# Optimization experiments

Measured on AMD Instinct MI355X. Metric: run time of the kernel, lower is better.

Reference implementation:

```python
import jax, jax.numpy as jnp
import numpy as np

N, T, D, H = 6144, 3072, 128, 4
ALPHA = 0.2
NEG = -9e15


def mhgat(x, mask, W, a_src, a_dst, fc_W, fc_b):
    # x: [n, D], mask: [n, n] (0/1), W: [H, D, D], a_src/a_dst: [H, D]
    Wh = jnp.einsum('nd,hde->hne', x, W)                      # [H, n, D]
    f_s = jnp.einsum('hne,he->hn', Wh, a_src)                 # [H, n]
    f_d = jnp.einsum('hne,he->hn', Wh, a_dst)                 # [H, n]
    e = jax.nn.leaky_relu(f_s[:, :, None] + f_d[:, None, :], ALPHA)  # [H, n, n]
    scores = jnp.where(mask[None, :, :] > 0, e, NEG)
    attn = jax.nn.softmax(scores, axis=-1)                    # masked softmax over neighbors
    h = jnp.einsum('hnm,hme->hne', attn, Wh)                  # [H, n, D]
    h = jax.nn.elu(h)                                         # concat=True -> elu per head
    h = jnp.transpose(h, (1, 0, 2)).reshape(x.shape[0], H * h.shape[-1])  # [n, H*D]
    return jax.nn.relu(h @ fc_W + fc_b)                       # fully_connectedLyer = Linear+ReLU


def setup_inputs() -> dict:
    key = jax.random.key(0)
    ks = jax.random.split(key, 20)
    s = 0.05
    return {
        'x': jax.random.normal(ks[0], (N, D), jnp.float32),
        'adj': jax.random.randint(ks[1], (N, N), 0, 2, jnp.int32),
        't_x': jax.random.normal(ks[2], (T, D), jnp.float32),
        't_adj': jax.random.randint(ks[3], (T, T), 0, 2, jnp.int32),
        'tfidf_x': jax.random.uniform(ks[4], (T, N), jnp.float32),
        # concept-graph MHGAT params
        'Wg': jax.random.normal(ks[5], (H, D, D), jnp.float32) * s,
        'ag_src': jax.random.normal(ks[6], (H, D), jnp.float32) * s,
        'ag_dst': jax.random.normal(ks[7], (H, D), jnp.float32) * s,
        'fcg_W': jax.random.normal(ks[8], (H * D, D), jnp.float32) * s,
        'fcg_b': jnp.zeros((D,), jnp.float32),
        # text-graph MHGAT params
        'Wt': jax.random.normal(ks[9], (H, D, D), jnp.float32) * s,
        'at_src': jax.random.normal(ks[10], (H, D), jnp.float32) * s,
        'at_dst': jax.random.normal(ks[11], (H, D), jnp.float32) * s,
        'fct_W': jax.random.normal(ks[12], (H * D, D), jnp.float32) * s,
        'fct_b': jnp.zeros((D,), jnp.float32),
        # fusion fc params
        'fus_W': jax.random.normal(ks[13], (D, D), jnp.float32) * s,
        'fus_b': jnp.zeros((D,), jnp.float32),
    }


def reference(x, adj, t_x, t_adj, tfidf_x,
              Wg, ag_src, ag_dst, fcg_W, fcg_b,
              Wt, at_src, at_dst, fct_W, fct_b,
              fus_W, fus_b):
    concept = mhgat(x, adj, Wg, ag_src, ag_dst, fcg_W, fcg_b)        # [N, D]
    gat_text = mhgat(t_x, t_adj, Wt, at_src, at_dst, fct_W, fct_b)   # [T, D]
    c_text = tfidf_x.T @ gat_text                                    # [N, D]
    z = jax.nn.sigmoid(concept + c_text)
    fusion = z * concept + (1.0 - z) * c_text
    return jax.nn.relu(fusion @ fus_W + fus_b)
```

## Files before the change

kernel.cpp:

```cpp
#include <hip/hip_runtime.h>
#include <hip/hip_bf16.h>
#include <stdint.h>

#define N_  6144
#define T_  3072
#define D_  128
#define H_  4
#define HD_ 512

typedef float f32x4 __attribute__((ext_vector_type(4)));
typedef short s16x8 __attribute__((ext_vector_type(8)));
typedef _Float16 h16x4 __attribute__((ext_vector_type(4)));

#define GLL16(g, s) __builtin_amdgcn_global_load_lds( \
    (const __attribute__((address_space(1))) unsigned int*)(g), \
    (__attribute__((address_space(3))) unsigned int*)(s), 16, 0, 0)

static __device__ __forceinline__ short f2bf(float f) {
  union { __hip_bfloat16 b; short s; } u;
  u.b = __float2bfloat16(f);
  return u.s;
}

__global__ __launch_bounds__(256) void bits8_kernel(const int* __restrict__ a0,
                                                    const int* __restrict__ a1,
                                                    unsigned long long* __restrict__ b0,
                                                    unsigned long long* __restrict__ b1,
                                                    int nw0, int nw1) {
  int lane = threadIdx.x & 63;
  int gw = (blockIdx.x * blockDim.x + threadIdx.x) >> 6;
  int nw = (gridDim.x * blockDim.x) >> 6;
  int total8 = (nw0 + nw1) >> 3;
  for (int g = gw; g < total8; g += nw) {
    int w = g * 8;
    const int* src; unsigned long long* dst; long wi;
    if (w < nw0) { src = a0; dst = b0; wi = w; }
    else         { src = a1; dst = b1; wi = w - nw0; }
    int v[8];
#pragma unroll
    for (int j = 0; j < 8; ++j) v[j] = src[(wi + j) * 64 + lane];
    unsigned long long bb[8];
#pragma unroll
    for (int j = 0; j < 8; ++j) bb[j] = __ballot(v[j] != 0);
    if (lane == 0) {
      ulonglong2 s01 = {bb[0], bb[1]}, s23 = {bb[2], bb[3]};
      ulonglong2 s45 = {bb[4], bb[5]}, s67 = {bb[6], bb[7]};
      *(ulonglong2*)(dst + wi + 0) = s01;
      *(ulonglong2*)(dst + wi + 2) = s23;
      *(ulonglong2*)(dst + wi + 4) = s45;
      *(ulonglong2*)(dst + wi + 6) = s67;
    }
  }
}

__global__ __launch_bounds__(256) void cvt2_kernel(const float* __restrict__ in0,
                                                   short* __restrict__ out0,
                                                   const float* __restrict__ in1,
                                                   short* __restrict__ out1,
                                                   int c0, int c1) {
  int i = blockIdx.x * blockDim.x + threadIdx.x;
  const float* in; short* out; long ii;
  if (i < c0) { in = in0; out = out0; ii = i; }
  else if (i < c0 + c1) { in = in1; out = out1; ii = i - c0; }
  else return;
  float4 v = *(const float4*)(in + ii * 4);
  short4 o;
  o.x = f2bf(v.x); o.y = f2bf(v.y); o.z = f2bf(v.z); o.w = f2bf(v.w);
  *(short4*)(out + ii * 4) = o;
}

__global__ __launch_bounds__(256) void tcvt2_kernel(const float* __restrict__ in0,
                                                    short* __restrict__ out0,
                                                    const float* __restrict__ in1,
                                                    short* __restrict__ out1,
                                                    int R, int C, long sIn, long sOut,
                                                    int zsplit) {
  __shared__ float t[32][33];
  const float* in; short* out;
  int z = blockIdx.z;
  if (z < zsplit) { in = in0 + (long)z * sIn; out = out0 + (long)z * sOut; }
  else            { in = in1 + (long)(z - zsplit) * sIn; out = out1 + (long)(z - zsplit) * sOut; }
  int c0 = blockIdx.x * 32, r0 = blockIdx.y * 32;
  int tx = threadIdx.x, ty = threadIdx.y;
#pragma unroll
  for (int i = 0; i < 4; ++i)
    t[ty + 8 * i][tx] = in[(long)(r0 + ty + 8 * i) * C + c0 + tx];
  __syncthreads();
#pragma unroll
  for (int i = 0; i < 4; ++i)
    out[(long)(c0 + ty + 8 * i) * R + r0 + tx] = f2bf(t[tx][ty + 8 * i]);
}

__global__ __launch_bounds__(256) void fvec_kernel(const float* __restrict__ x,
                                                   const float* __restrict__ W,
                                                   const float* __restrict__ a_s,
                                                   const float* __restrict__ a_d,
                                                   float* __restrict__ ea, float* __restrict__ ec,
                                                   float* __restrict__ inv,
                                                   float* __restrict__ eb, float* __restrict__ ed,
                                                   int n) {
  __shared__ float usl[128], udl[128], asl[128], adl[128];
  long idx = (long)blockIdx.x * 256 + threadIdx.x;
  int h = (int)(idx / n), i = (int)(idx % n);
  int tid = threadIdx.x;
  if (tid < 128) {
    asl[tid] = a_s[h * D_ + tid];
    adl[tid] = a_d[h * D_ + tid];
  }
  __syncthreads();
  {
    int d = tid & 127;
    const float* wr = W + ((long)h * D_ + d) * D_;
    const float* av = (tid < 128) ? asl : adl;
    float s = 0.f;
#pragma unroll 8
    for (int e = 0; e < D_; ++e) s += wr[e] * av[e];
    if (tid < 128) usl[d] = s; else udl[d] = s;
  }
  __syncthreads();
  const float4* xr = (const float4*)(x + (long)i * D_);
  float s = 0.f, t = 0.f;
#pragma unroll 8
  for (int e4 = 0; e4 < 32; ++e4) {
    float4 xv = xr[e4];
    s += xv.x * usl[4 * e4] + xv.y * usl[4 * e4 + 1] + xv.z * usl[4 * e4 + 2] + xv.w * usl[4 * e4 + 3];
    t += xv.x * udl[4 * e4] + xv.y * udl[4 * e4 + 1] + xv.z * udl[4 * e4 + 2] + xv.w * udl[4 * e4 + 3];
  }
  const float L2E = 1.4426950408889634f;
  float fs = s * L2E, fd = t * L2E;
  ea[idx]  = exp2f(fs);
  ec[idx]  = exp2f(0.2f * fs);
  inv[idx] = exp2f(-fs);
  eb[idx]  = exp2f(fd);
  ed[idx]  = exp2f(0.2f * fd);
}

__global__ __launch_bounds__(256) void gemm_kernel(const short* __restrict__ A,
                                                   const short* __restrict__ BT,
                                                   int K, int lda, int ldb,
                                                   float* __restrict__ outF, short* __restrict__ outB,
                                                   int ldo, int epi,
                                                   long sA, long sBT, long sOut) {
  int bz = blockIdx.z;
  A += bz * sA;
  BT += bz * sBT;
  __shared__ __align__(16) short bs[2][4096];
  int tid = threadIdx.x, w = tid >> 6, l = tid & 63, lm = l & 15, lg = l >> 4;
  int row0 = blockIdx.x * 64 + w * 16;
  int col0 = blockIdx.y * 128;
  const short* arow = A + (long)(row0 + lm) * lda + 8 * lg;
  const short* bsrc = BT + (long)(col0 + 16 * (2 * w) + lm) * ldb + 8 * lg;
  f32x4 acc[8] = {};
  int nt = K / 32;
  s16x8 af = *(const s16x8*)(arow);
  GLL16(bsrc, &bs[0][(2 * w) * 512]);
  GLL16(bsrc + 16 * ldb, &bs[0][(2 * w + 1) * 512]);
  for (int kt = 0; kt < nt; ++kt) {
    int cur = kt & 1, nxt = cur ^ 1;
    int kb = (kt + 1 < nt ? kt + 1 : kt) * 32;
    s16x8 an = *(const s16x8*)(arow + kb);
    asm volatile("s_waitcnt vmcnt(1)" ::: "memory");
    __builtin_amdgcn_sched_barrier(0);
    __builtin_amdgcn_s_barrier();
    __builtin_amdgcn_sched_barrier(0);
#pragma unroll
    for (int f = 0; f < 8; ++f) {
      s16x8 bf = *(const s16x8*)(&bs[cur][f * 512 + l * 8]);
      acc[f] = __builtin_amdgcn_mfma_f32_16x16x32_bf16(af, bf, acc[f], 0, 0, 0);
    }
    if (kt + 1 < nt) {
      GLL16(bsrc + kb, &bs[nxt][(2 * w) * 512]);
      GLL16(bsrc + kb + 16 * ldb, &bs[nxt][(2 * w + 1) * 512]);
    }
    __builtin_amdgcn_sched_barrier(0);
    af = an;
  }
#pragma unroll
  for (int f = 0; f < 8; ++f) {
    int col = col0 + 16 * f + lm;
#pragma unroll
    for (int r = 0; r < 4; ++r) {
      int row = row0 + 4 * lg + r;
      if (epi == 0) outB[bz * sOut + (long)row * ldo + col] = f2bf(acc[f][r]);
      else          outF[bz * sOut + (long)row * ldo + col] = acc[f][r];
    }
  }
}

__global__ __launch_bounds__(256) void reduce_kernel(const float* __restrict__ P,
                                                     int S, long sP,
                                                     const float* __restrict__ bias,
                                                     short* __restrict__ outB,
                                                     int ldo) {
  __shared__ short sm[128][68];
  int tid = threadIdx.x;
  int r0 = blockIdx.x * 64;
#pragma unroll
  for (int k = 0; k < 8; ++k) {
    int e = tid * 4 + k * 1024;
    int row = e >> 7, col = e & 127;
    f32x4 v = {};
    for (int s = 0; s < S; ++s)
      v += *(const f32x4*)(P + (long)s * sP + (long)(r0 + row) * 128 + col);
    const float4 bv = *(const float4*)(bias + col);
    v[0] += bv.x; v[1] += bv.y; v[2] += bv.z; v[3] += bv.w;
#pragma unroll
    for (int q = 0; q < 4; ++q) v[q] = v[q] > 0.f ? v[q] : 0.f;
    sm[col + 0][row] = f2bf(v[0]);
    sm[col + 1][row] = f2bf(v[1]);
    sm[col + 2][row] = f2bf(v[2]);
    sm[col + 3][row] = f2bf(v[3]);
  }
  __syncthreads();
  int d = tid >> 1, seg = tid & 1;
  short* dst = outB + (long)d * ldo + r0 + seg * 32;
#pragma unroll
  for (int q = 0; q < 8; ++q) {
    short4 o;
    o.x = sm[d][seg * 32 + 4 * q + 0];
    o.y = sm[d][seg * 32 + 4 * q + 1];
    o.z = sm[d][seg * 32 + 4 * q + 2];
    o.w = sm[d][seg * 32 + 4 * q + 3];
    *(short4*)(dst + 4 * q) = o;
  }
}

__global__ __launch_bounds__(256) void attn_kernel(const short* __restrict__ WhT,
                                                   const unsigned char* __restrict__ bits,
                                                   const float* __restrict__ eaA,
                                                   const float* __restrict__ ecA,
                                                   const float* __restrict__ invA,
                                                   const float* __restrict__ ebA,
                                                   const float* __restrict__ edA,
                                                   _Float16* __restrict__ pacc,
                                                   float* __restrict__ pz,
                                                   int n, int S) {
  int h = blockIdx.y, sp = blockIdx.z;
  int RB = gridDim.x;
  int klen = n / S, k0 = sp * klen;
  const short* whT = WhT + (long)h * D_ * n;
  const float* ebp = ebA + (long)h * n;
  const float* edp = edA + (long)h * n;
  __shared__ __align__(16) short bs[2][4096];
  int tid = threadIdx.x, w = tid >> 6, l = tid & 63, lm = l & 15, lg = l >> 4;
  int i0 = blockIdx.x * 128;
  int r0 = i0 + 32 * w + lm;
  int r1 = r0 + 16;
  float ea0 = eaA[(long)h * n + r0], ea1 = eaA[(long)h * n + r1];
  float ec0 = ecA[(long)h * n + r0], ec1 = ecA[(long)h * n + r1];
  float iv0 = invA[(long)h * n + r0], iv1 = invA[(long)h * n + r1];
  const unsigned char* brow0 = bits + (long)r0 * (n >> 3);
  const unsigned char* brow1 = bits + (long)r1 * (n >> 3);
  const short* bsrc = whT + (long)(16 * (2 * w) + lm) * n + 8 * lg + k0;
  f32x4 acc0[8] = {}, acc1[8] = {};
  f32x4 az0 = {}, az1 = {};
  s16x8 ones;
#pragma unroll
  for (int j = 0; j < 8; ++j) ones[j] = (short)0x3F80;
  int nt = klen / 32;
  float ebR[8], edR[8], ebS[8], edS[8];
  unsigned m0A, m1A, m0B, m1B;
  *(float4*)(ebR)     = *(const float4*)(ebp + k0 + 8 * lg);
  *(float4*)(ebR + 4) = *(const float4*)(ebp + k0 + 8 * lg + 4);
  *(float4*)(edR)     = *(const float4*)(edp + k0 + 8 * lg);
  *(float4*)(edR + 4) = *(const float4*)(edp + k0 + 8 * lg + 4);
  m0A = (*(const unsigned*)(brow0 + (k0 >> 3))) >> (8 * lg);
  m1A = (*(const unsigned*)(brow1 + (k0 >> 3))) >> (8 * lg);
  GLL16(bsrc, &bs[0][(2 * w) * 512]);
  GLL16(bsrc + 16 * n, &bs[0][(2 * w + 1) * 512]);

#define ATTN_STEP(KT, EBC, EDC, M0C, M1C, EBN, EDN, M0N, M1N)                   \
  {                                                                             \
    int cur = (KT) & 1, nxt = cur ^ 1;                                          \
    int kb = ((KT) + 1 < nt ? (KT) + 1 : (KT)) * 32;                            \
    *(float4*)(EBN)     = *(const float4*)(ebp + k0 + kb + 8 * lg);             \
    *(float4*)(EBN + 4) = *(const float4*)(ebp + k0 + kb + 8 * lg + 4);         \
    *(float4*)(EDN)     = *(const float4*)(edp + k0 + kb + 8 * lg);             \
    *(float4*)(EDN + 4) = *(const float4*)(edp + k0 + kb + 8 * lg + 4);         \
    M0N = (*(const unsigned*)(brow0 + ((k0 + kb) >> 3))) >> (8 * lg);           \
    M1N = (*(const unsigned*)(brow1 + ((k0 + kb) >> 3))) >> (8 * lg);           \
    union { s16x8 v; unsigned u[4]; } af0, af1;                                 \
    _Pragma("unroll")                                                           \
    for (int jj = 0; jj < 4; ++jj) {                                            \
      float bva = EBC[2 * jj], bvb = EBC[2 * jj + 1];                           \
      float dva = EDC[2 * jj], dvb = EDC[2 * jj + 1];                           \
      int ta = ((int)(M0C << (31 - 2 * jj))) >> 31;                             \
      int tb = ((int)(M0C << (30 - 2 * jj))) >> 31;                             \
      bool ca = bva > iv0, cb = bvb > iv0;                                      \
      float pa = (ca ? bva : dva) * (ca ? ea0 : ec0);                           \
      float pb = (cb ? bvb : dvb) * (cb ? ea0 : ec0);                           \
      pa = __int_as_float(ta & __float_as_int(pa));                             \
      pb = __int_as_float(tb & __float_as_int(pb));                             \
      af0.u[jj] = __builtin_amdgcn_perm(__float_as_uint(pb) + 0x8000u,          \
                                        __float_as_uint(pa) + 0x8000u, 0x07060302); \
      ta = ((int)(M1C << (31 - 2 * jj))) >> 31;                                 \
      tb = ((int)(M1C << (30 - 2 * jj))) >> 31;                                 \
      ca = bva > iv1; cb = bvb > iv1;                                           \
      pa = (ca ? bva : dva) * (ca ? ea1 : ec1);                                 \
      pb = (cb ? bvb : dvb) * (cb ? ea1 : ec1);                                 \
      pa = __int_as_float(ta & __float_as_int(pa));                             \
      pb = __int_as_float(tb & __float_as_int(pb));                             \
      af1.u[jj] = __builtin_amdgcn_perm(__float_as_uint(pb) + 0x8000u,          \
                                        __float_as_uint(pa) + 0x8000u, 0x07060302); \
    }                                                                           \
    asm volatile("s_waitcnt vmcnt(6)" ::: "memory");                            \
    __builtin_amdgcn_sched_barrier(0);                                          \
    __builtin_amdgcn_s_barrier();                                               \
    __builtin_amdgcn_sched_barrier(0);                                          \
    _Pragma("unroll")                                                           \
    for (int f = 0; f < 8; ++f) {                                               \
      s16x8 bf = *(const s16x8*)(&bs[cur][f * 512 + l * 8]);                    \
      acc0[f] = __builtin_amdgcn_mfma_f32_16x16x32_bf16(af0.v, bf, acc0[f], 0, 0, 0); \
      acc1[f] = __builtin_amdgcn_mfma_f32_16x16x32_bf16(af1.v, bf, acc1[f], 0, 0, 0); \
    }                                                                           \
    az0 = __builtin_amdgcn_mfma_f32_16x16x32_bf16(af0.v, ones, az0, 0, 0, 0);   \
    az1 = __builtin_amdgcn_mfma_f32_16x16x32_bf16(af1.v, ones, az1, 0, 0, 0);   \
    if ((KT) + 1 < nt) {                                                        \
      GLL16(bsrc + kb, &bs[nxt][(2 * w) * 512]);                                \
      GLL16(bsrc + kb + 16 * n, &bs[nxt][(2 * w + 1) * 512]);                   \
    }                                                                           \
    __builtin_amdgcn_sched_barrier(0);                                          \
  }

  for (int kt = 0; kt < nt; kt += 2) {
    ATTN_STEP(kt,     ebR, edR, m0A, m1A, ebS, edS, m0B, m1B);
    ATTN_STEP(kt + 1, ebS, edS, m0B, m1B, ebR, edR, m0A, m1A);
  }
#undef ATTN_STEP

  long base = (long)(h * RB + blockIdx.x) * S + sp;
  if (lm == 0) {
#pragma unroll
    for (int r = 0; r < 4; ++r) {
      pz[base * 128 + 32 * w + 4 * lg + r] = az0[r];
      pz[base * 128 + 32 * w + 16 + 4 * lg + r] = az1[r];
    }
  }
  long pb = base * 16384;
#pragma unroll
  for (int f = 0; f < 8; ++f)
#pragma unroll
    for (int r = 0; r < 4; ++r) {
      pacc[pb + (long)(32 * w + 4 * lg + r) * 128 + 16 * f + lm] = (_Float16)acc0[f][r];
      pacc[pb + (long)(32 * w + 16 + 4 * lg + r) * 128 + 16 * f + lm] = (_Float16)acc1[f][r];
    }
}

__global__ __launch_bounds__(256) void attn_combine_kernel(const _Float16* __restrict__ pacc,
                                                           const float* __restrict__ pz,
                                                           short* __restrict__ hcat,
                                                           int S) {
  int h = blockIdx.y, rb = blockIdx.x;
  int RB = gridDim.x;
  long base = (long)(h * RB + rb) * S;
  __shared__ float zl[128];
  int tid = threadIdx.x;
  if (tid < 128) {
    float zv = 0.f;
    for (int s = 0; s < S; ++s) zv += pz[(base + s) * 128 + tid];
    zl[tid] = 1.f / zv;
  }
  __syncthreads();
  int i0 = rb * 128;
#pragma unroll
  for (int k = 0; k < 16; ++k) {
    int e = tid * 4 + k * 1024;
    int row = e >> 7, col = e & 127;
    f32x4 v = {};
    for (int s = 0; s < S; ++s) {
      h16x4 hv = *(const h16x4*)(pacc + (base + s) * 16384 + e);
      v[0] += (float)hv[0]; v[1] += (float)hv[1];
      v[2] += (float)hv[2]; v[3] += (float)hv[3];
    }
    float iz = zl[row];
    short4 o;
    float t;
    t = v[0] * iz; o.x = f2bf(t > 0.f ? t : __expf(t) - 1.f);
    t = v[1] * iz; o.y = f2bf(t > 0.f ? t : __expf(t) - 1.f);
    t = v[2] * iz; o.z = f2bf(t > 0.f ? t : __expf(t) - 1.f);
    t = v[3] * iz; o.w = f2bf(t > 0.f ? t : __expf(t) - 1.f);
    *(short4*)(hcat + (long)(i0 + row) * HD_ + h * D_ + col) = o;
  }
}

__global__ __launch_bounds__(256) void fusion_kernel(const float* __restrict__ fcPg,
                                                     int Sf, long sPg,
                                                     const float* __restrict__ fcg_b,
                                                     const float* __restrict__ ctextP,
                                                     int Sc, long sCt,
                                                     const short* __restrict__ fusT,
                                                     const float* __restrict__ fus_b,
                                                     float* __restrict__ out) {
  __shared__ __align__(16) short als[64 * 136];
  int tid = threadIdx.x;
  int r0 = blockIdx.x * 64;
#pragma unroll
  for (int it = 0; it < 8; ++it) {
    int e = it * 1024 + tid * 4;
    int r = e >> 7, c = e & 127;
    f32x4 cv = {};
    for (int s = 0; s < Sf; ++s)
      cv += *(const f32x4*)(fcPg + (long)s * sPg + (long)(r0 + r) * D_ + c);
    const float4 bv = *(const float4*)(fcg_b + c);
    cv[0] += bv.x; cv[1] += bv.y; cv[2] += bv.z; cv[3] += bv.w;
#pragma unroll
    for (int q = 0; q < 4; ++q) cv[q] = cv[q] > 0.f ? cv[q] : 0.f;
    f32x4 tv = {};
    for (int s = 0; s < Sc; ++s)
      tv += *(const f32x4*)(ctextP + (long)s * sCt + (long)(r0 + r) * D_ + c);
    short4 o;
    {
      float s0 = cv[0] + tv[0]; float z = 1.f / (1.f + __expf(-s0)); o.x = f2bf(tv[0] + z * (cv[0] - tv[0]));
      s0 = cv[1] + tv[1]; z = 1.f / (1.f + __expf(-s0)); o.y = f2bf(tv[1] + z * (cv[1] - tv[1]));
      s0 = cv[2] + tv[2]; z = 1.f / (1.f + __expf(-s0)); o.z = f2bf(tv[2] + z * (cv[2] - tv[2]));
      s0 = cv[3] + tv[3]; z = 1.f / (1.f + __expf(-s0)); o.w = f2bf(tv[3] + z * (cv[3] - tv[3]));
    }
    *(short4*)(als + (long)r * 136 + c) = o;
  }
  __syncthreads();
  int w = tid >> 6, l = tid & 63, lm = l & 15, lg = l >> 4;
  f32x4 acc[8] = {};
#pragma unroll
  for (int kt = 0; kt < 4; ++kt) {
    int kb = kt * 32;
    s16x8 af = *(const s16x8*)(als + (16 * w + lm) * 136 + kb + 8 * lg);
#pragma unroll
    for (int f = 0; f < 8; ++f) {
      s16x8 bf = *(const s16x8*)(fusT + (long)(16 * f + lm) * D_ + kb + 8 * lg);
      acc[f] = __builtin_amdgcn_mfma_f32_16x16x32_bf16(af, bf, acc[f], 0, 0, 0);
    }
  }
#pragma unroll
  for (int f = 0; f < 8; ++f) {
    int col = 16 * f + lm;
#pragma unroll
    for (int r = 0; r < 4; ++r) {
      float v = acc[f][r] + fus_b[col];
      v = v > 0.f ? v : 0.f;
      out[(long)(r0 + 16 * w + 4 * lg + r) * D_ + col] = v;
    }
  }
}

extern "C" void kernel_launch(void* const* d_in, const int* in_sizes, int n_in,
                              void* d_out, int out_size, void* d_ws, size_t ws_size,
                              hipStream_t stream) {
  (void)in_sizes; (void)n_in; (void)out_size;
  const float* x      = (const float*)d_in[0];
  const int*   adj    = (const int*)d_in[1];
  const float* t_x    = (const float*)d_in[2];
  const int*   t_adj  = (const int*)d_in[3];
  const float* tfidf  = (const float*)d_in[4];
  const float* Wg     = (const float*)d_in[5];
  const float* ag_src = (const float*)d_in[6];
  const float* ag_dst = (const float*)d_in[7];
  const float* fcg_W  = (const float*)d_in[8];
  const float* fcg_b  = (const float*)d_in[9];
  const float* Wt     = (const float*)d_in[10];
  const float* at_src = (const float*)d_in[11];
  const float* at_dst = (const float*)d_in[12];
  const float* fct_W  = (const float*)d_in[13];
  const float* fct_b  = (const float*)d_in[14];
  const float* fus_W  = (const float*)d_in[15];
  const float* fus_b  = (const float*)d_in[16];
  float* out = (float*)d_out;

  char* ws = (char*)d_ws;
  size_t off = 0;
  auto alloc = [&](size_t bytes) -> char* {
    char* p = ws + off;
    off = (off + bytes + 255) & ~(size_t)255;
    return p;
  };
  unsigned long long* bitsG = (unsigned long long*)alloc((size_t)N_ * N_ / 8);
  unsigned long long* bitsT = (unsigned long long*)alloc((size_t)T_ * T_ / 8);
  short* xb     = (short*)alloc((size_t)N_ * D_ * 2);
  short* txb    = (short*)alloc((size_t)T_ * D_ * 2);
  short* WgT    = (short*)alloc((size_t)H_ * D_ * D_ * 2);
  short* WtT    = (short*)alloc((size_t)H_ * D_ * D_ * 2);
  short* fcgT   = (short*)alloc((size_t)HD_ * D_ * 2);
  short* fctT   = (short*)alloc((size_t)HD_ * D_ * 2);
  short* fusT   = (short*)alloc((size_t)D_ * D_ * 2);
  short* tfidfT = (short*)alloc((size_t)N_ * T_ * 2);
  short* WhTg   = (short*)alloc((size_t)H_ * D_ * N_ * 2);
  short* WhTt   = (short*)alloc((size_t)H_ * D_ * T_ * 2);
  float* eaG  = (float*)alloc((size_t)H_ * N_ * 4);
  float* ecG  = (float*)alloc((size_t)H_ * N_ * 4);
  float* invG = (float*)alloc((size_t)H_ * N_ * 4);
  float* ebG  = (float*)alloc((size_t)H_ * N_ * 4);
  float* edG  = (float*)alloc((size_t)H_ * N_ * 4);
  float* eaT  = (float*)alloc((size_t)H_ * T_ * 4);
  float* ecT  = (float*)alloc((size_t)H_ * T_ * 4);
  float* invT = (float*)alloc((size_t)H_ * T_ * 4);
  float* ebT  = (float*)alloc((size_t)H_ * T_ * 4);
  float* edT  = (float*)alloc((size_t)H_ * T_ * 4);
  short* hcatG = (short*)alloc((size_t)N_ * HD_ * 2);
  short* hcatT = (short*)alloc((size_t)T_ * HD_ * 2);
  short* gatT  = (short*)alloc((size_t)D_ * T_ * 2);

  const int RBg = N_ / 128, RBt = T_ / 128;
  const size_t paccG1 = (size_t)H_ * RBg * 16384 * 2;
  const size_t paccT1 = (size_t)H_ * RBt * 16384 * 2;
  const size_t pzG1   = (size_t)H_ * RBg * 128 * 4;
  const size_t pzT1   = (size_t)H_ * RBt * 128 * 4;
  const size_t fcPg1  = (size_t)N_ * D_ * 4;
  const size_t fcPt1  = (size_t)T_ * D_ * 4;
  const size_t ctp1   = (size_t)N_ * D_ * 4;
  size_t rem = (ws_size > off + (1 << 20)) ? (ws_size - off - (1 << 20)) : 0;
  int Sg = 2, St = 2, Sf = 1, Sc = 1;
  size_t needFull = 8 * (paccG1 + pzG1) + 8 * (paccT1 + pzT1) + 4 * fcPg1 + 4 * fcPt1 + 4 * ctp1;
  size_t needMid  = 4 * (paccG1 + pzG1) + 4 * (paccT1 + pzT1) + 2 * fcPg1 + 2 * fcPt1 + 2 * ctp1;
  if (rem >= needFull)      { Sg = 8; St = 8; Sf = 4; Sc = 4; }
  else if (rem >= needMid)  { Sg = 4; St = 4; Sf = 2; Sc = 2; }
  _Float16* paccG = (_Float16*)alloc(Sg * paccG1);
  float* pzG   = (float*)alloc(Sg * pzG1);
  _Float16* paccT = (_Float16*)alloc(St * paccT1);
  float* pzT   = (float*)alloc(St * pzT1);
  float* fcPg  = (float*)alloc(Sf * fcPg1);
  float* fcPt  = (float*)alloc(Sf * fcPt1);
  float* ctextP = (float*)alloc(Sc * ctp1);

  bits8_kernel<<<dim3(1536), dim3(256), 0, stream>>>(adj, t_adj, bitsG, bitsT,
                                                     N_ * N_ / 64, T_ * T_ / 64);
  cvt2_kernel<<<dim3((N_ + T_) * D_ / 1024), dim3(256), 0, stream>>>(
      x, xb, t_x, txb, N_ * D_ / 4, T_ * D_ / 4);
  tcvt2_kernel<<<dim3(4, 4, 8), dim3(32, 8), 0, stream>>>(
      Wg, WgT, Wt, WtT, D_, D_, (long)D_ * D_, (long)D_ * D_, 4);
  tcvt2_kernel<<<dim3(4, 16, 2), dim3(32, 8), 0, stream>>>(
      fcg_W, fcgT, fct_W, fctT, HD_, D_, 0, 0, 1);
  tcvt2_kernel<<<dim3(4, 4, 1), dim3(32, 8), 0, stream>>>(
      fus_W, fusT, fus_W, fusT, D_, D_, 0, 0, 1);
  tcvt2_kernel<<<dim3(N_ / 32, T_ / 32, 1), dim3(32, 8), 0, stream>>>(
      tfidf, tfidfT, tfidf, tfidfT, T_, N_, 0, 0, 1);
  fvec_kernel<<<dim3(H_ * N_ / 256), dim3(256), 0, stream>>>(
      x, Wg, ag_src, ag_dst, eaG, ecG, invG, ebG, edG, N_);
  fvec_kernel<<<dim3(H_ * T_ / 256), dim3(256), 0, stream>>>(
      t_x, Wt, at_src, at_dst, eaT, ecT, invT, ebT, edT, T_);

  gemm_kernel<<<dim3(2, N_ / 128, H_), dim3(256), 0, stream>>>(
      WgT, xb, D_, D_, D_, nullptr, WhTg, N_, 0, (long)D_ * D_, 0, (long)D_ * N_);
  gemm_kernel<<<dim3(2, T_ / 128, H_), dim3(256), 0, stream>>>(
      WtT, txb, D_, D_, D_, nullptr, WhTt, T_, 0, (long)D_ * D_, 0, (long)D_ * T_);

  attn_kernel<<<dim3(RBg, H_, Sg), dim3(256), 0, stream>>>(
      WhTg, (const unsigned char*)bitsG, eaG, ecG, invG, ebG, edG, paccG, pzG, N_, Sg);
  attn_combine_kernel<<<dim3(RBg, H_), dim3(256), 0, stream>>>(paccG, pzG, hcatG, Sg);
  attn_kernel<<<dim3(RBt, H_, St), dim3(256), 0, stream>>>(
      WhTt, (const unsigned char*)bitsT, eaT, ecT, invT, ebT, edT, paccT, pzT, T_, St);
  attn_combine_kernel<<<dim3(RBt, H_), dim3(256), 0, stream>>>(paccT, pzT, hcatT, St);

  gemm_kernel<<<dim3(N_ / 64, 1, Sf), dim3(256), 0, stream>>>(
      hcatG, fcgT, HD_ / Sf, HD_, HD_, fcPg, nullptr, D_, 3,
      (long)(HD_ / Sf), (long)(HD_ / Sf), (long)N_ * D_);
  gemm_kernel<<<dim3(T_ / 64, 1, Sf), dim3(256), 0, stream>>>(
      hcatT, fctT, HD_ / Sf, HD_, HD_, fcPt, nullptr, D_, 3,
      (long)(HD_ / Sf), (long)(HD_ / Sf), (long)T_ * D_);
  reduce_kernel<<<dim3(T_ / 64), dim3(256), 0, stream>>>(
      fcPt, Sf, (long)T_ * D_, fct_b, gatT, T_);

  gemm_kernel<<<dim3(N_ / 64, 1, Sc), dim3(256), 0, stream>>>(
      tfidfT, gatT, T_ / Sc, T_, T_, ctextP, nullptr, D_, 3,
      (long)(T_ / Sc), (long)(T_ / Sc), (long)N_ * D_);

  fusion_kernel<<<dim3(N_ / 64), dim3(256), 0, stream>>>(
      fcPg, Sf, (long)N_ * D_, fcg_b, ctextP, Sc, (long)N_ * D_, fusT, fus_b, out);
}
```

Measured before the change: 392.4 us.

## Switch pipeline to fp16 MFMA with packed-half attention weights and triple buffering

Converts all bf16 intermediates and MFMA calls to fp16. The attention weight computation now uses packed half-precision multiply and max (max(ea*eb, ec*ed) replacing the compare-and-select leaky-relu), which drops the inv array and halves eb/ed storage. The gemm and attention kernels move from double to triple buffering with two-ahead global-to-LDS prefetch. Split-K factors are also changed. This carries fp16 overflow/precision risk for the exponentials and uses more shared memory per block.

```diff
diff --git a/kernel.cpp b/kernel.cpp
--- a/kernel.cpp
+++ b/kernel.cpp
@@ -9,17 +9,32 @@
 #define HD_ 512
 
 typedef float f32x4 __attribute__((ext_vector_type(4)));
-typedef short s16x8 __attribute__((ext_vector_type(8)));
+typedef _Float16 f16x8 __attribute__((ext_vector_type(8)));
 typedef _Float16 h16x4 __attribute__((ext_vector_type(4)));
 
 #define GLL16(g, s) __builtin_amdgcn_global_load_lds( \
     (const __attribute__((address_space(1))) unsigned int*)(g), \
     (__attribute__((address_space(3))) unsigned int*)(s), 16, 0, 0)
 
-static __device__ __forceinline__ short f2bf(float f) {
-  union { __hip_bfloat16 b; short s; } u;
-  u.b = __float2bfloat16(f);
+static __device__ __forceinline__ short f2h(float f) {
+  union { _Float16 h; short s; } u;
+  u.h = (_Float16)f;
   return u.s;
+}
+static __device__ __forceinline__ unsigned pk2(float f) {
+  union { _Float16 h[2]; unsigned u; } t;
+  t.h[0] = (_Float16)f; t.h[1] = t.h[0];
+  return t.u;
+}
+static __device__ __forceinline__ unsigned pkmul(unsigned a, unsigned b) {
+  unsigned r;
+  asm("v_pk_mul_f16 %0, %1, %2" : "=v"(r) : "v"(a), "v"(b));
+  return r;
+}
+static __device__ __forceinline__ unsigned pkmax(unsigned a, unsigned b) {
+  unsigned r;
+  asm("v_pk_max_f16 %0, %1, %2" : "=v"(r) : "v"(a), "v"(b));
+  return r;
 }
 
 __global__ __launch_bounds__(256) void bits8_kernel(const int* __restrict__ a0,
@@ -65,7 +80,7 @@
   else return;
   float4 v = *(const float4*)(in + ii * 4);
   short4 o;
-  o.x = f2bf(v.x); o.y = f2bf(v.y); o.z = f2bf(v.z); o.w = f2bf(v.w);
+  o.x = f2h(v.x); o.y = f2h(v.y); o.z = f2h(v.z); o.w = f2h(v.w);
   *(short4*)(out + ii * 4) = o;
 }
 
@@ -88,7 +103,7 @@
   __syncthreads();
 #pragma unroll
   for (int i = 0; i < 4; ++i)
-    out[(long)(c0 + ty + 8 * i) * R + r0 + tx] = f2bf(t[tx][ty + 8 * i]);
+    out[(long)(c0 + ty + 8 * i) * R + r0 + tx] = f2h(t[tx][ty + 8 * i]);
 }
 
 __global__ __launch_bounds__(256) void fvec_kernel(const float* __restrict__ x,
@@ -96,8 +111,7 @@
                                                    const float* __restrict__ a_s,
                                                    const float* __restrict__ a_d,
                                                    float* __restrict__ ea, float* __restrict__ ec,
-                                                   float* __restrict__ inv,
-                                                   float* __restrict__ eb, float* __restrict__ ed,
+                                                   short* __restrict__ ebh, short* __restrict__ edh,
                                                    int n) {
   __shared__ float usl[128], udl[128], asl[128], adl[128];
   long idx = (long)blockIdx.x * 256 + threadIdx.x;
@@ -130,9 +144,8 @@
   float fs = s * L2E, fd = t * L2E;
   ea[idx]  = exp2f(fs);
   ec[idx]  = exp2f(0.2f * fs);
-  inv[idx] = exp2f(-fs);
-  eb[idx]  = exp2f(fd);
-  ed[idx]  = exp2f(0.2f * fd);
+  ebh[idx] = f2h(exp2f(fd));
+  edh[idx] = f2h(exp2f(0.2f * fd));
 }
 
 __global__ __launch_bounds__(256) void gemm_kernel(const short* __restrict__ A,
@@ -144,7 +157,7 @@
   int bz = blockIdx.z;
   A += bz * sA;
   BT += bz * sBT;
-  __shared__ __align__(16) short bs[2][4096];
+  __shared__ __align__(16) short bs[3][4096];
   int tid = threadIdx.x, w = tid >> 6, l = tid & 63, lm = l & 15, lg = l >> 4;
   int row0 = blockIdx.x * 64 + w * 16;
   int col0 = blockIdx.y * 128;
@@ -152,25 +165,29 @@
   const short* bsrc = BT + (long)(col0 + 16 * (2 * w) + lm) * ldb + 8 * lg;
   f32x4 acc[8] = {};
   int nt = K / 32;
-  s16x8 af = *(const s16x8*)(arow);
+  f16x8 af = *(const f16x8*)(arow);
   GLL16(bsrc, &bs[0][(2 * w) * 512]);
   GLL16(bsrc + 16 * ldb, &bs[0][(2 * w + 1) * 512]);
+  GLL16(bsrc + 32, &bs[1][(2 * w) * 512]);
+  GLL16(bsrc + 32 + 16 * ldb, &bs[1][(2 * w + 1) * 512]);
   for (int kt = 0; kt < nt; ++kt) {
-    int cur = kt & 1, nxt = cur ^ 1;
+    int cur = kt % 3;
     int kb = (kt + 1 < nt ? kt + 1 : kt) * 32;
-    s16x8 an = *(const s16x8*)(arow + kb);
-    asm volatile("s_waitcnt vmcnt(1)" ::: "memory");
+    f16x8 an = *(const f16x8*)(arow + kb);
+    asm volatile("s_waitcnt vmcnt(3)" ::: "memory");
     __builtin_amdgcn_sched_barrier(0);
     __builtin_amdgcn_s_barrier();
     __builtin_amdgcn_sched_barrier(0);
 #pragma unroll
     for (int f = 0; f < 8; ++f) {
-      s16x8 bf = *(const s16x8*)(&bs[cur][f * 512 + l * 8]);
-      acc[f] = __builtin_amdgcn_mfma_f32_16x16x32_bf16(af, bf, acc[f], 0, 0, 0);
-    }
-    if (kt + 1 < nt) {
-      GLL16(bsrc + kb, &bs[nxt][(2 * w) * 512]);
-      GLL16(bsrc + kb + 16 * ldb, &bs[nxt][(2 * w + 1) * 512]);
+      f16x8 bf = *(const f16x8*)(&bs[cur][f * 512 + l * 8]);
+      acc[f] = __builtin_amdgcn_mfma_f32_16x16x32_f16(af, bf, acc[f], 0, 0, 0);
+    }
+    {
+      int kg = (kt + 2 < nt ? kt + 2 : nt - 1) * 32;
+      int tb = (kt + 2) % 3;
+      GLL16(bsrc + kg, &bs[tb][(2 * w) * 512]);
+      GLL16(bsrc + kg + 16 * ldb, &bs[tb][(2 * w + 1) * 512]);
     }
     __builtin_amdgcn_sched_barrier(0);
     af = an;
@@ -181,7 +198,7 @@
 #pragma unroll
     for (int r = 0; r < 4; ++r) {
       int row = row0 + 4 * lg + r;
-      if (epi == 0) outB[bz * sOut + (long)row * ldo + col] = f2bf(acc[f][r]);
+      if (epi == 0) outB[bz * sOut + (long)row * ldo + col] = f2h(acc[f][r]);
       else          outF[bz * sOut + (long)row * ldo + col] = acc[f][r];
     }
   }
@@ -206,10 +223,10 @@
     v[0] += bv.x; v[1] += bv.y; v[2] += bv.z; v[3] += bv.w;
 #pragma unroll
     for (int q = 0; q < 4; ++q) v[q] = v[q] > 0.f ? v[q] : 0.f;
-    sm[col + 0][row] = f2bf(v[0]);
-    sm[col + 1][row] = f2bf(v[1]);
-    sm[col + 2][row] = f2bf(v[2]);
-    sm[col + 3][row] = f2bf(v[3]);
+    sm[col + 0][row] = f2h(v[0]);
+    sm[col + 1][row] = f2h(v[1]);
+    sm[col + 2][row] = f2h(v[2]);
+    sm[col + 3][row] = f2h(v[3]);
   }
   __syncthreads();
   int d = tid >> 1, seg = tid & 1;
@@ -229,9 +246,8 @@
                                                    const unsigned char* __restrict__ bits,
                                                    const float* __restrict__ eaA,
                                                    const float* __restrict__ ecA,
-                                                   const float* __restrict__ invA,
-                                                   const float* __restrict__ ebA,
-                                                   const float* __restrict__ edA,
+                                                   const short* __restrict__ ebA,
+                                                   const short* __restrict__ edA,
                                                    _Float16* __restrict__ pacc,
                                                    float* __restrict__ pz,
                                                    int n, int S) {
@@ -239,69 +255,54 @@
   int RB = gridDim.x;
   int klen = n / S, k0 = sp * klen;
   const short* whT = WhT + (long)h * D_ * n;
-  const float* ebp = ebA + (long)h * n;
-  const float* edp = edA + (long)h * n;
-  __shared__ __align__(16) short bs[2][4096];
+  const short* ebp = ebA + (long)h * n;
+  const short* edp = edA + (long)h * n;
+  __shared__ __align__(16) short bs[3][4096];
   int tid = threadIdx.x, w = tid >> 6, l = tid & 63, lm = l & 15, lg = l >> 4;
   int i0 = blockIdx.x * 128;
   int r0 = i0 + 32 * w + lm;
   int r1 = r0 + 16;
-  float ea0 = eaA[(long)h * n + r0], ea1 = eaA[(long)h * n + r1];
-  float ec0 = ecA[(long)h * n + r0], ec1 = ecA[(long)h * n + r1];
-  float iv0 = invA[(long)h * n + r0], iv1 = invA[(long)h * n + r1];
+  unsigned ea0p = pk2(eaA[(long)h * n + r0]), ea1p = pk2(eaA[(long)h * n + r1]);
+  unsigned ec0p = pk2(ecA[(long)h * n + r0]), ec1p = pk2(ecA[(long)h * n + r1]);
   const unsigned char* brow0 = bits + (long)r0 * (n >> 3);
   const unsigned char* brow1 = bits + (long)r1 * (n >> 3);
   const short* bsrc = whT + (long)(16 * (2 * w) + lm) * n + 8 * lg + k0;
   f32x4 acc0[8] = {}, acc1[8] = {};
   f32x4 az0 = {}, az1 = {};
-  s16x8 ones;
-#pragma unroll
-  for (int j = 0; j < 8; ++j) ones[j] = (short)0x3F80;
+  f16x8 ones;
+#pragma unroll
+  for (int j = 0; j < 8; ++j) ones[j] = (_Float16)1.0f;
   int nt = klen / 32;
-  float ebR[8], edR[8], ebS[8], edS[8];
+  unsigned ebR[4], edR[4], ebS[4], edS[4];
   unsigned m0A, m1A, m0B, m1B;
-  *(float4*)(ebR)     = *(const float4*)(ebp + k0 + 8 * lg);
-  *(float4*)(ebR + 4) = *(const float4*)(ebp + k0 + 8 * lg + 4);
-  *(float4*)(edR)     = *(const float4*)(edp + k0 + 8 * lg);
-  *(float4*)(edR + 4) = *(const float4*)(edp + k0 + 8 * lg + 4);
+  *(uint4*)(ebR) = *(const uint4*)(ebp + k0 + 8 * lg);
+  *(uint4*)(edR) = *(const uint4*)(edp + k0 + 8 * lg);
   m0A = (*(const unsigned*)(brow0 + (k0 >> 3))) >> (8 * lg);
   m1A = (*(const unsigned*)(brow1 + (k0 >> 3))) >> (8 * lg);
   GLL16(bsrc, &bs[0][(2 * w) * 512]);
   GLL16(bsrc + 16 * n, &bs[0][(2 * w + 1) * 512]);
+  GLL16(bsrc + 32, &bs[1][(2 * w) * 512]);
+  GLL16(bsrc + 32 + 16 * n, &bs[1][(2 * w + 1) * 512]);
 
 #define ATTN_STEP(KT, EBC, EDC, M0C, M1C, EBN, EDN, M0N, M1N)                   \
   {                                                                             \
-    int cur = (KT) & 1, nxt = cur ^ 1;                                          \
+    int cur = (KT) % 3;                                                         \
     int kb = ((KT) + 1 < nt ? (KT) + 1 : (KT)) * 32;                            \
-    *(float4*)(EBN)     = *(const float4*)(ebp + k0 + kb + 8 * lg);             \
-    *(float4*)(EBN + 4) = *(const float4*)(ebp + k0 + kb + 8 * lg + 4);         \
-    *(float4*)(EDN)     = *(const float4*)(edp + k0 + kb + 8 * lg);             \
-    *(float4*)(EDN + 4) = *(const float4*)(edp + k0 + kb + 8 * lg + 4);         \
+    *(uint4*)(EBN) = *(const uint4*)(ebp + k0 + kb + 8 * lg);                   \
+    *(uint4*)(EDN) = *(const uint4*)(edp + k0 + kb + 8 * lg);                   \
     M0N = (*(const unsigned*)(brow0 + ((k0 + kb) >> 3))) >> (8 * lg);           \
     M1N = (*(const unsigned*)(brow1 + ((k0 + kb) >> 3))) >> (8 * lg);           \
-    union { s16x8 v; unsigned u[4]; } af0, af1;                                 \
+    union { f16x8 v; unsigned u[4]; } af0, af1;                                 \
     _Pragma("unroll")                                                           \
     for (int jj = 0; jj < 4; ++jj) {                                            \
-      float bva = EBC[2 * jj], bvb = EBC[2 * jj + 1];                           \
-      float dva = EDC[2 * jj], dvb = EDC[2 * jj + 1];                           \
+      unsigned pm0 = pkmax(pkmul(ea0p, EBC[jj]), pkmul(ec0p, EDC[jj]));         \
+      unsigned pm1 = pkmax(pkmul(ea1p, EBC[jj]), pkmul(ec1p, EDC[jj]));         \
       int ta = ((int)(M0C << (31 - 2 * jj))) >> 31;                             \
       int tb = ((int)(M0C << (30 - 2 * jj))) >> 31;                             \
-      bool ca = bva > iv0, cb = bvb > iv0;                                      \
-      float pa = (ca ? bva : dva) * (ca ? ea0 : ec0);                           \
-      float pb = (cb ? bvb : dvb) * (cb ? ea0 : ec0);                           \
-      pa = __int_as_float(ta & __float_as_int(pa));                             \
-      pb = __int_as_float(tb & __float_as_int(pb));                             \
-      af0.u[jj] = __builtin_amdgcn_perm(__float_as_uint(pb) + 0x8000u,          \
-                                        __float_as_uint(pa) + 0x8000u, 0x07060302); \
+      af0.u[jj] = pm0 & __builtin_amdgcn_perm((unsigned)tb, (unsigned)ta, 0x07060302u); \
       ta = ((int)(M1C << (31 - 2 * jj))) >> 31;                                 \
       tb = ((int)(M1C << (30 - 2 * jj))) >> 31;                                 \
-      ca = bva > iv1; cb = bvb > iv1;                                           \
-      pa = (ca ? bva : dva) * (ca ? ea1 : ec1);                                 \
-      pb = (cb ? bvb : dvb) * (cb ? ea1 : ec1);                                 \
-      pa = __int_as_float(ta & __float_as_int(pa));                             \
-      pb = __int_as_float(tb & __float_as_int(pb));                             \
-      af1.u[jj] = __builtin_amdgcn_perm(__float_as_uint(pb) + 0x8000u,          \
-                                        __float_as_uint(pa) + 0x8000u, 0x07060302); \
+      af1.u[jj] = pm1 & __builtin_amdgcn_perm((unsigned)tb, (unsigned)ta, 0x07060302u); \
     }                                                                           \
     asm volatile("s_waitcnt vmcnt(6)" ::: "memory");                            \
     __builtin_amdgcn_sched_barrier(0);                                          \
@@ -309,15 +310,17 @@
     __builtin_amdgcn_sched_barrier(0);                                          \
     _Pragma("unroll")                                                           \
     for (int f = 0; f < 8; ++f) {                                               \
-      s16x8 bf = *(const s16x8*)(&bs[cur][f * 512 + l * 8]);                    \
-      acc0[f] = __builtin_amdgcn_mfma_f32_16x16x32_bf16(af0.v, bf, acc0[f], 0, 0, 0); \
-      acc1[f] = __builtin_amdgcn_mfma_f32_16x16x32_bf16(af1.v, bf, acc1[f], 0, 0, 0); \
+      f16x8 bf = *(const f16x8*)(&bs[cur][f * 512 + l * 8]);                    \
+      acc0[f] = __builtin_amdgcn_mfma_f32_16x16x32_f16(af0.v, bf, acc0[f], 0, 0, 0); \
+      acc1[f] = __builtin_amdgcn_mfma_f32_16x16x32_f16(af1.v, bf, acc1[f], 0, 0, 0); \
     }                                                                           \
-    az0 = __builtin_amdgcn_mfma_f32_16x16x32_bf16(af0.v, ones, az0, 0, 0, 0);   \
-    az1 = __builtin_amdgcn_mfma_f32_16x16x32_bf16(af1.v, ones, az1, 0, 0, 0);   \
-    if ((KT) + 1 < nt) {                                                        \
-      GLL16(bsrc + kb, &bs[nxt][(2 * w) * 512]);                                \
-      GLL16(bsrc + kb + 16 * n, &bs[nxt][(2 * w + 1) * 512]);                   \
+    az0 = __builtin_amdgcn_mfma_f32_16x16x32_f16(af0.v, ones, az0, 0, 0, 0);    \
+    az1 = __builtin_amdgcn_mfma_f32_16x16x32_f16(af1.v, ones, az1, 0, 0, 0);    \
+    {                                                                           \
+      int kg = ((KT) + 2 < nt ? (KT) + 2 : nt - 1) * 32;                        \
+      int tb2 = ((KT) + 2) % 3;                                                 \
+      GLL16(bsrc + kg, &bs[tb2][(2 * w) * 512]);                                \
+      GLL16(bsrc + kg + 16 * n, &bs[tb2][(2 * w + 1) * 512]);                   \
     }                                                                           \
     __builtin_amdgcn_sched_barrier(0);                                          \
   }
@@ -375,10 +378,10 @@
     float iz = zl[row];
     short4 o;
     float t;
-    t = v[0] * iz; o.x = f2bf(t > 0.f ? t : __expf(t) - 1.f);
-    t = v[1] * iz; o.y = f2bf(t > 0.f ? t : __expf(t) - 1.f);
-    t = v[2] * iz; o.z = f2bf(t > 0.f ? t : __expf(t) - 1.f);
-    t = v[3] * iz; o.w = f2bf(t > 0.f ? t : __expf(t) - 1.f);
+    t = v[0] * iz; o.x = f2h(t > 0.f ? t : __expf(t) - 1.f);
+    t = v[1] * iz; o.y = f2h(t > 0.f ? t : __expf(t) - 1.f);
+    t = v[2] * iz; o.z = f2h(t > 0.f ? t : __expf(t) - 1.f);
+    t = v[3] * iz; o.w = f2h(t > 0.f ? t : __expf(t) - 1.f);
     *(short4*)(hcat + (long)(i0 + row) * HD_ + h * D_ + col) = o;
   }
 }
@@ -410,10 +413,10 @@
       tv += *(const f32x4*)(ctextP + (long)s * sCt + (long)(r0 + r) * D_ + c);
     short4 o;
     {
-      float s0 = cv[0] + tv[0]; float z = 1.f / (1.f + __expf(-s0)); o.x = f2bf(tv[0] + z * (cv[0] - tv[0]));
-      s0 = cv[1] + tv[1]; z = 1.f / (1.f + __expf(-s0)); o.y = f2bf(tv[1] + z * (cv[1] - tv[1]));
-      s0 = cv[2] + tv[2]; z = 1.f / (1.f + __expf(-s0)); o.z = f2bf(tv[2] + z * (cv[2] - tv[2]));
-      s0 = cv[3] + tv[3]; z = 1.f / (1.f + __expf(-s0)); o.w = f2bf(tv[3] + z * (cv[3] - tv[3]));
+      float s0 = cv[0] + tv[0]; float z = 1.f / (1.f + __expf(-s0)); o.x = f2h(tv[0] + z * (cv[0] - tv[0]));
+      s0 = cv[1] + tv[1]; z = 1.f / (1.f + __expf(-s0)); o.y = f2h(tv[1] + z * (cv[1] - tv[1]));
+      s0 = cv[2] + tv[2]; z = 1.f / (1.f + __expf(-s0)); o.z = f2h(tv[2] + z * (cv[2] - tv[2]));
+      s0 = cv[3] + tv[3]; z = 1.f / (1.f + __expf(-s0)); o.w = f2h(tv[3] + z * (cv[3] - tv[3]));
     }
     *(short4*)(als + (long)r * 136 + c) = o;
   }
@@ -423,11 +426,11 @@
 #pragma unroll
   for (int kt = 0; kt < 4; ++kt) {
     int kb = kt * 32;
-    s16x8 af = *(const s16x8*)(als + (16 * w + lm) * 136 + kb + 8 * lg);
+    f16x8 af = *(const f16x8*)(als + (16 * w + lm) * 136 + kb + 8 * lg);
 #pragma unroll
     for (int f = 0; f < 8; ++f) {
-      s16x8 bf = *(const s16x8*)(fusT + (long)(16 * f + lm) * D_ + kb + 8 * lg);
-      acc[f] = __builtin_amdgcn_mfma_f32_16x16x32_bf16(af, bf, acc[f], 0, 0, 0);
+      f16x8 bf = *(const f16x8*)(fusT + (long)(16 * f + lm) * D_ + kb + 8 * lg);
+      acc[f] = __builtin_amdgcn_mfma_f32_16x16x32_f16(af, bf, acc[f], 0, 0, 0);
     }
   }
 #pragma unroll
@@ -486,14 +489,12 @@
   short* WhTt   = (short*)alloc((size_t)H_ * D_ * T_ * 2);
   float* eaG  = (float*)alloc((size_t)H_ * N_ * 4);
   float* ecG  = (float*)alloc((size_t)H_ * N_ * 4);
-  float* invG = (float*)alloc((size_t)H_ * N_ * 4);
-  float* ebG  = (float*)alloc((size_t)H_ * N_ * 4);
-  float* edG  = (float*)alloc((size_t)H_ * N_ * 4);
+  short* ebG  = (short*)alloc((size_t)H_ * N_ * 2);
+  short* edG  = (short*)alloc((size_t)H_ * N_ * 2);
   float* eaT  = (float*)alloc((size_t)H_ * T_ * 4);
   float* ecT  = (float*)alloc((size_t)H_ * T_ * 4);
-  float* invT = (float*)alloc((size_t)H_ * T_ * 4);
-  float* ebT  = (float*)alloc((size_t)H_ * T_ * 4);
-  float* edT  = (float*)alloc((size_t)H_ * T_ * 4);
+  short* ebT  = (short*)alloc((size_t)H_ * T_ * 2);
+  short* edT  = (short*)alloc((size_t)H_ * T_ * 2);
   short* hcatG = (short*)alloc((size_t)N_ * HD_ * 2);
   short* hcatT = (short*)alloc((size_t)T_ * HD_ * 2);
   short* gatT  = (short*)alloc((size_t)D_ * T_ * 2);
@@ -507,11 +508,9 @@
   const size_t fcPt1  = (size_t)T_ * D_ * 4;
   const size_t ctp1   = (size_t)N_ * D_ * 4;
   size_t rem = (ws_size > off + (1 << 20)) ? (ws_size - off - (1 << 20)) : 0;
-  int Sg = 2, St = 2, Sf = 1, Sc = 1;
-  size_t needFull = 8 * (paccG1 + pzG1) + 8 * (paccT1 + pzT1) + 4 * fcPg1 + 4 * fcPt1 + 4 * ctp1;
-  size_t needMid  = 4 * (paccG1 + pzG1) + 4 * (paccT1 + pzT1) + 2 * fcPg1 + 2 * fcPt1 + 2 * ctp1;
-  if (rem >= needFull)      { Sg = 8; St = 8; Sf = 4; Sc = 4; }
-  else if (rem >= needMid)  { Sg = 4; St = 4; Sf = 2; Sc = 2; }
+  int Sg = 2, St = 2, Sf = 2, Sc = 2;
+  size_t needFull = 4 * (paccG1 + pzG1) + 4 * (paccT1 + pzT1) + 4 * fcPg1 + 4 * fcPt1 + 4 * ctp1;
+  if (rem >= needFull) { Sg = 4; St = 4; Sf = 4; Sc = 4; }
   _Float16* paccG = (_Float16*)alloc(Sg * paccG1);
   float* pzG   = (float*)alloc(Sg * pzG1);
   _Float16* paccT = (_Float16*)alloc(St * paccT1);
@@ -533,9 +532,9 @@
   tcvt2_kernel<<<dim3(N_ / 32, T_ / 32, 1), dim3(32, 8), 0, stream>>>(
       tfidf, tfidfT, tfidf, tfidfT, T_, N_, 0, 0, 1);
   fvec_kernel<<<dim3(H_ * N_ / 256), dim3(256), 0, stream>>>(
-      x, Wg, ag_src, ag_dst, eaG, ecG, invG, ebG, edG, N_);
+      x, Wg, ag_src, ag_dst, eaG, ecG, ebG, edG, N_);
   fvec_kernel<<<dim3(H_ * T_ / 256), dim3(256), 0, stream>>>(
-      t_x, Wt, at_src, at_dst, eaT, ecT, invT, ebT, edT, T_);
+      t_x, Wt, at_src, at_dst, eaT, ecT, ebT, edT, T_);
 
   gemm_kernel<<<dim3(2, N_ / 128, H_), dim3(256), 0, stream>>>(
       WgT, xb, D_, D_, D_, nullptr, WhTg, N_, 0, (long)D_ * D_, 0, (long)D_ * N_);
@@ -543,10 +542,10 @@
       WtT, txb, D_, D_, D_, nullptr, WhTt, T_, 0, (long)D_ * D_, 0, (long)D_ * T_);
 
   attn_kernel<<<dim3(RBg, H_, Sg), dim3(256), 0, stream>>>(
-      WhTg, (const unsigned char*)bitsG, eaG, ecG, invG, ebG, edG, paccG, pzG, N_, Sg);
+      WhTg, (const unsigned char*)bitsG, eaG, ecG, ebG, edG, paccG, pzG, N_, Sg);
   attn_combine_kernel<<<dim3(RBg, H_), dim3(256), 0, stream>>>(paccG, pzG, hcatG, Sg);
   attn_kernel<<<dim3(RBt, H_, St), dim3(256), 0, stream>>>(
-      WhTt, (const unsigned char*)bitsT, eaT, ecT, invT, ebT, edT, paccT, pzT, T_, St);
+      WhTt, (const unsigned char*)bitsT, eaT, ecT, ebT, edT, paccT, pzT, T_, St);
   attn_combine_kernel<<<dim3(RBt, H_), dim3(256), 0, stream>>>(paccT, pzT, hcatT, St);
 
   gemm_kernel<<<dim3(N_ / 64, 1, Sf), dim3(256), 0, stream>>>(
```

New measurement: 365.2 us. 6.9% less time.
